# Kernel optimization log

Measured on AMD Instinct MI355X. Metric: run time of the kernel, lower is better.

The kernel has to match this reference:

```python
import jax, jax.numpy as jnp
import numpy as np

B, C, H, W = 4, 3, 256, 256
NCC = 64            # num_conv_channels
N_HIDDEN = 20 - 2   # hidden_block applied num_hiddel_blocks-2 times (shared weights)
EPS = 1e-5          # BatchNorm eps (eval mode: running stats; Dropout2d is identity in eval)


def _bayer_mask():
    # RGGB Bayer pattern: each channel sampled only at its sites, zeros elsewhere
    m = np.zeros((3, H, W), dtype=np.float32)
    m[0, 0::2, 0::2] = 1.0  # R
    m[1, 0::2, 1::2] = 1.0  # G
    m[1, 1::2, 0::2] = 1.0  # G
    m[2, 1::2, 1::2] = 1.0  # B
    return jnp.asarray(m)


def setup_inputs() -> dict:
    key = jax.random.key(0)
    ks = jax.random.split(key, 8)
    X = jax.random.uniform(ks[0], (B, C, H, W), dtype=jnp.float32) * _bayer_mask()[None]
    w_in = jax.random.normal(ks[1], (NCC, 3, 3, 3), dtype=jnp.float32) * 0.15
    b_in = jnp.zeros((NCC,), jnp.float32)
    w_h = jax.random.normal(ks[2], (NCC, NCC, 3, 3), dtype=jnp.float32) * 0.04
    b_h = jnp.zeros((NCC,), jnp.float32)
    w_out = jax.random.normal(ks[3], (3, NCC, 3, 3), dtype=jnp.float32) * 0.04
    b_out = jnp.zeros((3,), jnp.float32)
    def bn_params(n):
        return (jnp.ones((n,), jnp.float32), jnp.zeros((n,), jnp.float32),
                jnp.zeros((n,), jnp.float32), jnp.ones((n,), jnp.float32))
    g_in, be_in, m_in, v_in = bn_params(NCC)
    g_h, be_h, m_h, v_h = bn_params(NCC)
    g_out, be_out, m_out, v_out = bn_params(3)
    return dict(X=X, w_in=w_in, b_in=b_in, g_in=g_in, be_in=be_in, m_in=m_in, v_in=v_in,
                w_h=w_h, b_h=b_h, g_h=g_h, be_h=be_h, m_h=m_h, v_h=v_h,
                w_out=w_out, b_out=b_out, g_out=g_out, be_out=be_out, m_out=m_out, v_out=v_out)


def _conv(x, w, b):
    y = jax.lax.conv_general_dilated(x, w, (1, 1), ((1, 1), (1, 1)),
                                     dimension_numbers=('NCHW', 'OIHW', 'NCHW'))
    return y + b[None, :, None, None]


def _bn(x, g, be, m, v):
    scale = (g / jnp.sqrt(v + EPS))[None, :, None, None]
    return (x - m[None, :, None, None]) * scale + be[None, :, None, None]


def _interpolate_zeros(x):
    # Vectorized masked cross-neighbor average at zero sites, dividing by the
    # count of strictly-positive neighbors (zero-padded borders).
    p = jnp.pad(x, ((0, 0), (0, 0), (1, 1), (1, 1)))
    left = p[:, :, 1:-1, :-2]
    right = p[:, :, 1:-1, 2:]
    top = p[:, :, :-2, 1:-1]
    bottom = p[:, :, 2:, 1:-1]
    nb_sum = left + right + top + bottom
    nb_cnt = ((left > 0).astype(x.dtype) + (right > 0).astype(x.dtype)
              + (top > 0).astype(x.dtype) + (bottom > 0).astype(x.dtype))
    mean = jnp.where(nb_cnt > 0, nb_sum / jnp.maximum(nb_cnt, 1.0), 0.0)
    return jnp.where(x == 0, mean, x)


def reference(X, w_in, b_in, g_in, be_in, m_in, v_in,
              w_h, b_h, g_h, be_h, m_h, v_h,
              w_out, b_out, g_out, be_out, m_out, v_out):
    y = jax.nn.selu(_bn(_conv(X, w_in, b_in), g_in, be_in, m_in, v_in))

    def hidden(y, _):
        y = jax.nn.selu(_bn(_conv(y, w_h, b_h), g_h, be_h, m_h, v_h))
        return y, None

    y, _ = jax.lax.scan(hidden, y, None, length=N_HIDDEN)
    y = jax.nn.selu(_bn(_conv(y, w_out, b_out), g_out, be_out, m_out, v_out))
    return y + _interpolate_zeros(X)
```

## Files before the change

### kernel.cpp

```cpp
#include <hip/hip_runtime.h>

#define EPS 1e-5f
#define SELU_L 1.0507009873554805f
#define SELU_A 1.6732632423543772f
#define SELU_LA (SELU_L * SELU_A)

typedef _Float16 half8 __attribute__((ext_vector_type(8)));
typedef _Float16 half4 __attribute__((ext_vector_type(4)));
typedef float floatx4 __attribute__((ext_vector_type(4)));

__device__ __forceinline__ float selu_f(float x) {
    return x > 0.f ? SELU_L * x : SELU_LA * (__expf(x) - 1.f);
}

__device__ __forceinline__ void gload_lds16(const _Float16* g, _Float16* l) {
    __builtin_amdgcn_global_load_lds(
        (const __attribute__((address_space(1))) void*)g,
        (__attribute__((address_space(3))) void*)l, 16, 0, 0);
}

__global__ __launch_bounds__(256) void k_prep(
    const float* __restrict__ w_h, const float* __restrict__ w_in,
    const float* __restrict__ w_out, _Float16* __restrict__ wb_h,
    _Float16* __restrict__ wb_in, _Float16* __restrict__ wb_out,
    _Float16* __restrict__ zp)
{
    int i = blockIdx.x * 256 + threadIdx.x;
    if (i < 256) zp[i] = (_Float16)0.f;
    if (i < 36864) {
        int t = i >> 11;
        int rem = i & 2047;
        int mi = rem >> 9;
        int L = (rem >> 3) & 63;
        int j = i & 7;
        int co = mi * 16 + (L & 15);
        int ci = ((t & 1) << 5) + ((L >> 4) << 3) + j;
        int s = t >> 1;
        wb_h[i] = (_Float16)w_h[(co * 64 + ci) * 9 + s];
    } else if (i < 36864 + 2048) {
        int e = i - 36864;
        int mi = e >> 9;
        int L = (e >> 3) & 63;
        int j = e & 7;
        int co = mi * 16 + (L & 15);
        int k = ((L >> 4) << 3) + j;
        _Float16 val = (_Float16)0.f;
        if (k < 27) {
            int s = k / 3, ci = k - s * 3;
            val = (_Float16)w_in[(co * 3 + ci) * 9 + s];
        }
        wb_in[e] = val;
    } else if (i < 36864 + 2048 + 9216) {
        int e = i - 36864 - 2048;
        int t = e >> 9;
        int L = (e >> 3) & 63;
        int j = e & 7;
        int co = L & 15;
        int ci = ((t & 1) << 5) + ((L >> 4) << 3) + j;
        int s = t >> 1;
        _Float16 val = (_Float16)0.f;
        if (co < 3) val = (_Float16)w_out[(co * 64 + ci) * 9 + s];
        wb_out[e] = val;
    }
}

__global__ __launch_bounds__(256) void k_conv_in_mfma(
    const float* __restrict__ X, const _Float16* __restrict__ wb,
    const float* __restrict__ bconv, const float* __restrict__ g,
    const float* __restrict__ be, const float* __restrict__ bm,
    const float* __restrict__ bv, _Float16* __restrict__ dst)
{
    __shared__ float s_x[3][18][18];
    __shared__ float s_sc[64], s_bs[64];
    const int tid = threadIdx.x;
    const int tau = ((blockIdx.x & 7) << 7) + (blockIdx.x >> 3);
    const int b = tau >> 8, rem = tau & 255;
    const int h0 = (rem >> 4) << 4, w0 = (rem & 15) << 4;

    if (tid < 64) {
        float sc = g[tid] * rsqrtf(bv[tid] + EPS);
        s_sc[tid] = sc;
        s_bs[tid] = (bconv[tid] - bm[tid]) * sc + be[tid];
    }
    for (int idx = tid; idx < 3 * 324; idx += 256) {
        int ci = idx / 324, rem2 = idx - ci * 324;
        int r = rem2 / 18, c = rem2 - r * 18;
        int gh = h0 - 1 + r, gw = w0 - 1 + c;
        float val = 0.f;
        if ((unsigned)gh < 256u && (unsigned)gw < 256u)
            val = X[((b * 3 + ci) << 16) + (gh << 8) + gw];
        s_x[ci][r][c] = val;
    }
    __syncthreads();

    const int wv = tid >> 6, L = tid & 63, quad = L >> 4, l15 = L & 15;
    half8 a[4];
    #pragma unroll
    for (int mi = 0; mi < 4; ++mi)
        a[mi] = *(const half8*)(wb + (mi * 64 + L) * 8);

    floatx4 acc[4][4];
    #pragma unroll
    for (int mi = 0; mi < 4; ++mi)
        #pragma unroll
        for (int ni = 0; ni < 4; ++ni) acc[mi][ni] = (floatx4){0.f, 0.f, 0.f, 0.f};

    #pragma unroll
    for (int ni = 0; ni < 4; ++ni) {
        half8 bfr;
        #pragma unroll
        for (int j = 0; j < 8; ++j) {
            int k = quad * 8 + j;
            float xv = 0.f;
            if (k < 27) {
                int s = k / 3, ci = k - s * 3;
                int kh = s / 3, kw = s - kh * 3;
                xv = s_x[ci][wv * 4 + ni + kh][l15 + kw];
            }
            bfr[j] = (_Float16)xv;
        }
        #pragma unroll
        for (int mi = 0; mi < 4; ++mi)
            acc[mi][ni] = __builtin_amdgcn_mfma_f32_16x16x32_f16(a[mi], bfr, acc[mi][ni], 0, 0, 0);
    }

    _Float16* db = dst + ((size_t)b << 22);
    #pragma unroll
    for (int mi = 0; mi < 4; ++mi) {
        const int cob = mi * 16 + quad * 4;
        floatx4 sc = *(const floatx4*)(&s_sc[cob]);
        floatx4 bs = *(const floatx4*)(&s_bs[cob]);
        #pragma unroll
        for (int ni = 0; ni < 4; ++ni) {
            half4 ov;
            #pragma unroll
            for (int r = 0; r < 4; ++r)
                ov[r] = (_Float16)selu_f(acc[mi][ni][r] * sc[r] + bs[r]);
            const int row = h0 + wv * 4 + ni, col = w0 + l15;
            *(half4*)(db + ((((row << 8) + col) << 6) + cob)) = ov;
        }
    }
}

__global__ __launch_bounds__(1024) void k_hidden_v14(
    const _Float16* __restrict__ src, const _Float16* __restrict__ wb,
    const float* __restrict__ bconv, const float* __restrict__ g,
    const float* __restrict__ be, const float* __restrict__ bm,
    const float* __restrict__ bv, const _Float16* __restrict__ zp,
    _Float16* __restrict__ dst)
{
    __shared__ _Float16 s_w[36864];
    __shared__ _Float16 s_act[2][20992];
    __shared__ float s_sc[64], s_bs[64];
    const int tid = threadIdx.x;
    const int wv = tid >> 6, L = tid & 63, quad = L >> 4, l15 = L & 15;
    const int rh = wv >> 1, mh = wv & 1;

    if (tid < 64) {
        float sc = g[tid] * rsqrtf(bv[tid] + EPS);
        s_sc[tid] = sc;
        s_bs[tid] = (bconv[tid] - bm[tid]) * sc + be[tid];
    }

    #pragma unroll
    for (int k = 0; k < 5; ++k) {
        const int wc = k * 16 + wv;
        if (wc < 72)
            gload_lds16(wb + ((wc << 6) + L) * 8, &s_w[wc << 9]);
    }

    auto stage = [&](int tau, int buf) {
        const int b = tau >> 8, rem = tau & 255;
        const int h0 = (rem >> 4) << 4, w0 = (rem & 15) << 4;
        const _Float16* sb = src + ((size_t)b << 22);
        #pragma unroll
        for (int k = 0; k < 3; ++k) {
            const int wc = k * 16 + wv;
            if (wc < 41) {
                const int p = (wc << 3) + (L >> 3);
                const int sd = (L & 7) ^ (p & 7);
                const int rp = p / 18, cl = p - rp * 18;
                const int gh = h0 - 1 + rp, gw = w0 - 1 + cl;
                const _Float16* gp = (p < 324 && (unsigned)gh < 256u && (unsigned)gw < 256u)
                    ? sb + ((((gh << 8) + gw) << 6) + (sd << 3)) : zp;
                gload_lds16(gp, &s_act[buf][wc << 9]);
            }
        }
    };

    const int swz = ((blockIdx.x & 7) << 5) + (blockIdx.x >> 3);
    const int tau0 = swz << 2;
    stage(tau0, 0);
    __syncthreads();

    for (int ti = 0; ti < 4; ++ti) {
        const int tau = tau0 + ti, cur = ti & 1;
        if (ti < 3) stage(tau + 1, cur ^ 1);

        floatx4 acc[2][2];
        #pragma unroll
        for (int m = 0; m < 2; ++m)
            #pragma unroll
            for (int ni = 0; ni < 2; ++ni) acc[m][ni] = (floatx4){0.f, 0.f, 0.f, 0.f};

        const _Float16* bufp = &s_act[cur][0];
        #pragma unroll
        for (int h = 0; h < 2; ++h) {
            const int sb8 = (h << 2) + quad;
            #pragma unroll
            for (int kw = 0; kw < 3; ++kw) {
                half8 ac[3][2];
                #pragma unroll
                for (int kh = 0; kh < 3; ++kh) {
                    const int t = ((kh * 3 + kw) << 1) + h;
                    ac[kh][0] = *(const half8*)(&s_w[((t * 4 + mh * 2 + 0) * 64 + L) * 8]);
                    ac[kh][1] = *(const half8*)(&s_w[((t * 4 + mh * 2 + 1) * 64 + L) * 8]);
                }
                #pragma unroll
                for (int j = 0; j < 4; ++j) {
                    const int p = (rh * 2 + j) * 18 + l15 + kw;
                    half8 bfr = *(const half8*)(bufp + (p << 6) + (((p & 7) ^ sb8) << 3));
                    #pragma unroll
                    for (int kh = 0; kh < 3; ++kh) {
                        const int ni = j - kh;
                        if (ni >= 0 && ni < 2) {
                            acc[0][ni] = __builtin_amdgcn_mfma_f32_16x16x32_f16(ac[kh][0], bfr, acc[0][ni], 0, 0, 0);
                            acc[1][ni] = __builtin_amdgcn_mfma_f32_16x16x32_f16(ac[kh][1], bfr, acc[1][ni], 0, 0, 0);
                        }
                    }
                }
            }
        }

        const int b = tau >> 8, rem = tau & 255;
        const int h0 = (rem >> 4) << 4, w0 = (rem & 15) << 4;
        _Float16* db = dst + ((size_t)b << 22);
        #pragma unroll
        for (int m = 0; m < 2; ++m) {
            const int cob = (mh * 2 + m) * 16 + quad * 4;
            floatx4 sc = *(const floatx4*)(&s_sc[cob]);
            floatx4 bs = *(const floatx4*)(&s_bs[cob]);
            #pragma unroll
            for (int ni = 0; ni < 2; ++ni) {
                half4 ov;
                #pragma unroll
                for (int r = 0; r < 4; ++r)
                    ov[r] = (_Float16)selu_f(acc[m][ni][r] * sc[r] + bs[r]);
                const int row = h0 + rh * 2 + ni, col = w0 + l15;
                *(half4*)(db + ((((row << 8) + col) << 6) + cob)) = ov;
            }
        }
        __syncthreads();
    }
}

__global__ __launch_bounds__(256) void k_conv_out_mfma(
    const _Float16* __restrict__ src, const _Float16* __restrict__ wb,
    const float* __restrict__ bconv, const float* __restrict__ g,
    const float* __restrict__ be, const float* __restrict__ bm,
    const float* __restrict__ bv, const float* __restrict__ X,
    float* __restrict__ out)
{
    __shared__ _Float16 s_in[324 * 72];
    const int tid = threadIdx.x;
    const int tau = ((blockIdx.x & 7) << 7) + (blockIdx.x >> 3);
    const int b = tau >> 8, rem = tau & 255;
    const int h0 = (rem >> 4) << 4, w0 = (rem & 15) << 4;
    const _Float16* sb = src + ((size_t)b << 22);

    for (int idx = tid; idx < 2592; idx += 256) {
        int r = idx / 144, cpos = idx - r * 144;
        int col = cpos >> 3, sub = cpos & 7;
        int gh = h0 - 1 + r, gw = w0 - 1 + col;
        half8 val = {0, 0, 0, 0, 0, 0, 0, 0};
        if ((unsigned)gh < 256u && (unsigned)gw < 256u)
            val = *(const half8*)(sb + ((((gh << 8) + gw) << 6) + (sub << 3)));
        *(half8*)(&s_in[(r * 18 + col) * 72 + (sub << 3)]) = val;
    }
    __syncthreads();

    const int wv = tid >> 6, L = tid & 63, quad = L >> 4, l15 = L & 15;
    floatx4 acc[4];
    #pragma unroll
    for (int ni = 0; ni < 4; ++ni) acc[ni] = (floatx4){0.f, 0.f, 0.f, 0.f};

    #pragma unroll
    for (int t = 0; t < 18; ++t) {
        const int s = t >> 1, ci0 = (t & 1) << 5;
        const int kh = s / 3, kw = s - kh * 3;
        half8 a = *(const half8*)(wb + (t * 64 + L) * 8);
        #pragma unroll
        for (int ni = 0; ni < 4; ++ni) {
            const int row = wv * 4 + ni + kh, col = l15 + kw;
            half8 bfr = *(const half8*)(&s_in[(row * 18 + col) * 72 + ci0 + quad * 8]);
            acc[ni] = __builtin_amdgcn_mfma_f32_16x16x32_f16(a, bfr, acc[ni], 0, 0, 0);
        }
    }

    if (quad == 0) {
        float sc[3], bs[3];
        #pragma unroll
        for (int co = 0; co < 3; ++co) {
            sc[co] = g[co] * rsqrtf(bv[co] + EPS);
            bs[co] = (bconv[co] - bm[co]) * sc[co] + be[co];
        }
        #pragma unroll
        for (int ni = 0; ni < 4; ++ni) {
            const int h = h0 + wv * 4 + ni, wc = w0 + l15;
            #pragma unroll
            for (int co = 0; co < 3; ++co) {
                float val = selu_f(acc[ni][co] * sc[co] + bs[co]);
                const float* Xc = X + ((size_t)(b * 3 + co) << 16);
                float x = Xc[(h << 8) + wc];
                float res;
                if (x == 0.f) {
                    float lft = (wc > 0)   ? Xc[(h << 8) + wc - 1] : 0.f;
                    float rgt = (wc < 255) ? Xc[(h << 8) + wc + 1] : 0.f;
                    float top = (h > 0)    ? Xc[((h - 1) << 8) + wc] : 0.f;
                    float bot = (h < 255)  ? Xc[((h + 1) << 8) + wc] : 0.f;
                    float sm = lft + rgt + top + bot;
                    int cnt = (lft > 0.f) + (rgt > 0.f) + (top > 0.f) + (bot > 0.f);
                    res = cnt > 0 ? sm / (float)cnt : 0.f;
                } else {
                    res = x;
                }
                out[((b * 3 + co) << 16) + (h << 8) + wc] = val + res;
            }
        }
    }
}

extern "C" void kernel_launch(void* const* d_in, const int* in_sizes, int n_in,
                              void* d_out, int out_size, void* d_ws, size_t ws_size,
                              hipStream_t stream) {
    (void)in_sizes; (void)n_in; (void)out_size; (void)ws_size;
    const float* X    = (const float*)d_in[0];
    const float* w_in = (const float*)d_in[1];
    const float* b_in = (const float*)d_in[2];
    const float* g_in = (const float*)d_in[3];
    const float* be_in= (const float*)d_in[4];
    const float* m_in = (const float*)d_in[5];
    const float* v_in = (const float*)d_in[6];
    const float* w_h  = (const float*)d_in[7];
    const float* b_h  = (const float*)d_in[8];
    const float* g_h  = (const float*)d_in[9];
    const float* be_h = (const float*)d_in[10];
    const float* m_h  = (const float*)d_in[11];
    const float* v_h  = (const float*)d_in[12];
    const float* w_o  = (const float*)d_in[13];
    const float* b_o  = (const float*)d_in[14];
    const float* g_o  = (const float*)d_in[15];
    const float* be_o = (const float*)d_in[16];
    const float* m_o  = (const float*)d_in[17];
    const float* v_o  = (const float*)d_in[18];
    float* out = (float*)d_out;

    _Float16* act0  = (_Float16*)d_ws;
    _Float16* act1  = act0 + ((size_t)1 << 24);
    _Float16* wb_h  = act1 + ((size_t)1 << 24);
    _Float16* wb_in = wb_h + 36864;
    _Float16* wb_out= wb_in + 2048;
    _Float16* zp    = wb_out + 9216;

    k_prep<<<188, 256, 0, stream>>>(w_h, w_in, w_o, wb_h, wb_in, wb_out, zp);
    k_conv_in_mfma<<<1024, 256, 0, stream>>>(X, wb_in, b_in, g_in, be_in, m_in, v_in, act0);
    _Float16* src = act0;
    _Float16* dst = act1;
    for (int i = 0; i < 18; ++i) {
        k_hidden_v14<<<256, 1024, 0, stream>>>(src, wb_h, b_h, g_h, be_h, m_h, v_h, zp, dst);
        _Float16* t = src; src = dst; dst = t;
    }
    k_conv_out_mfma<<<1024, 256, 0, stream>>>(src, wb_out, b_o, g_o, be_o, m_o, v_o, X, out);
}
```

Measured before the change: 553.2 us.

## Split hidden conv per output-channel half, one tile per block, 2 blocks/CU

Replaces the persistent 1024-thread hidden-layer kernel, which looped over four tiles with double-buffered LDS staging, with 2048 blocks of 512 threads. Each block handles one 16x16 tile and one half of the 64 output channels, so it loads only half the weights. Less LDS per block allows two resident blocks per CU, hiding load latency through occupancy rather than explicit double buffering. In exchange, each input tile halo is now staged twice (once per channel half), and weights are loaded per block, which raises global and L2 traffic.

```diff
diff --git a/kernel.cpp b/kernel.cpp
--- a/kernel.cpp
+++ b/kernel.cpp
@@ -142,19 +142,26 @@
     }
 }
 
-__global__ __launch_bounds__(1024) void k_hidden_v14(
+__global__ __launch_bounds__(512, 2) void k_hidden_v15(
     const _Float16* __restrict__ src, const _Float16* __restrict__ wb,
     const float* __restrict__ bconv, const float* __restrict__ g,
     const float* __restrict__ be, const float* __restrict__ bm,
     const float* __restrict__ bv, const _Float16* __restrict__ zp,
     _Float16* __restrict__ dst)
 {
-    __shared__ _Float16 s_w[36864];
-    __shared__ _Float16 s_act[2][20992];
+    __shared__ _Float16 s_w[18432];
+    __shared__ _Float16 s_act[20992];
     __shared__ float s_sc[64], s_bs[64];
     const int tid = threadIdx.x;
     const int wv = tid >> 6, L = tid & 63, quad = L >> 4, l15 = L & 15;
-    const int rh = wv >> 1, mh = wv & 1;
+    const int rq = wv;
+
+    const int xcd = blockIdx.x & 7, q = blockIdx.x >> 3;
+    const int hb = q & 1;
+    const int tau = (xcd << 7) + (q >> 1);
+    const int b = tau >> 8, rem = tau & 255;
+    const int h0 = (rem >> 4) << 4, w0 = (rem & 15) << 4;
+    const _Float16* sb = src + ((size_t)b << 22);
 
     if (tid < 64) {
         float sc = g[tid] * rsqrtf(bv[tid] + EPS);
@@ -164,93 +171,78 @@
 
     #pragma unroll
     for (int k = 0; k < 5; ++k) {
-        const int wc = k * 16 + wv;
-        if (wc < 72)
-            gload_lds16(wb + ((wc << 6) + L) * 8, &s_w[wc << 9]);
-    }
-
-    auto stage = [&](int tau, int buf) {
-        const int b = tau >> 8, rem = tau & 255;
-        const int h0 = (rem >> 4) << 4, w0 = (rem & 15) << 4;
-        const _Float16* sb = src + ((size_t)b << 22);
-        #pragma unroll
-        for (int k = 0; k < 3; ++k) {
-            const int wc = k * 16 + wv;
-            if (wc < 41) {
-                const int p = (wc << 3) + (L >> 3);
-                const int sd = (L & 7) ^ (p & 7);
-                const int rp = p / 18, cl = p - rp * 18;
-                const int gh = h0 - 1 + rp, gw = w0 - 1 + cl;
-                const _Float16* gp = (p < 324 && (unsigned)gh < 256u && (unsigned)gw < 256u)
-                    ? sb + ((((gh << 8) + gw) << 6) + (sd << 3)) : zp;
-                gload_lds16(gp, &s_act[buf][wc << 9]);
+        const int wcl = k * 8 + wv;
+        if (wcl < 36) {
+            const int t = wcl >> 1, m = wcl & 1;
+            const int wcg = (t << 2) + (hb << 1) + m;
+            gload_lds16(wb + ((wcg << 6) + L) * 8, &s_w[wcl << 9]);
+        }
+    }
+
+    #pragma unroll
+    for (int k = 0; k < 6; ++k) {
+        const int wc = k * 8 + wv;
+        if (wc < 41) {
+            const int p = (wc << 3) + (L >> 3);
+            const int sd = (L & 7) ^ (p & 7);
+            const int rp = p / 18, cl = p - rp * 18;
+            const int gh = h0 - 1 + rp, gw = w0 - 1 + cl;
+            const _Float16* gp = (p < 324 && (unsigned)gh < 256u && (unsigned)gw < 256u)
+                ? sb + ((((gh << 8) + gw) << 6) + (sd << 3)) : zp;
+            gload_lds16(gp, &s_act[wc << 9]);
+        }
+    }
+    __syncthreads();
+
+    floatx4 acc[2][2];
+    #pragma unroll
+    for (int m = 0; m < 2; ++m)
+        #pragma unroll
+        for (int ni = 0; ni < 2; ++ni) acc[m][ni] = (floatx4){0.f, 0.f, 0.f, 0.f};
+
+    #pragma unroll
+    for (int h = 0; h < 2; ++h) {
+        const int sb8 = (h << 2) + quad;
+        #pragma unroll
+        for (int kw = 0; kw < 3; ++kw) {
+            half8 ac[3][2];
+            #pragma unroll
+            for (int kh = 0; kh < 3; ++kh) {
+                const int t = ((kh * 3 + kw) << 1) + h;
+                ac[kh][0] = *(const half8*)(&s_w[((t * 2 + 0) * 64 + L) * 8]);
+                ac[kh][1] = *(const half8*)(&s_w[((t * 2 + 1) * 64 + L) * 8]);
             }
-        }
-    };
-
-    const int swz = ((blockIdx.x & 7) << 5) + (blockIdx.x >> 3);
-    const int tau0 = swz << 2;
-    stage(tau0, 0);
-    __syncthreads();
-
-    for (int ti = 0; ti < 4; ++ti) {
-        const int tau = tau0 + ti, cur = ti & 1;
-        if (ti < 3) stage(tau + 1, cur ^ 1);
-
-        floatx4 acc[2][2];
-        #pragma unroll
-        for (int m = 0; m < 2; ++m)
-            #pragma unroll
-            for (int ni = 0; ni < 2; ++ni) acc[m][ni] = (floatx4){0.f, 0.f, 0.f, 0.f};
-
-        const _Float16* bufp = &s_act[cur][0];
-        #pragma unroll
-        for (int h = 0; h < 2; ++h) {
-            const int sb8 = (h << 2) + quad;
-            #pragma unroll
-            for (int kw = 0; kw < 3; ++kw) {
-                half8 ac[3][2];
+            #pragma unroll
+            for (int j = 0; j < 4; ++j) {
+                const int p = (rq * 2 + j) * 18 + l15 + kw;
+                half8 bfr = *(const half8*)(&s_act[(p << 6) + (((p & 7) ^ sb8) << 3)]);
                 #pragma unroll
                 for (int kh = 0; kh < 3; ++kh) {
-                    const int t = ((kh * 3 + kw) << 1) + h;
-                    ac[kh][0] = *(const half8*)(&s_w[((t * 4 + mh * 2 + 0) * 64 + L) * 8]);
-                    ac[kh][1] = *(const half8*)(&s_w[((t * 4 + mh * 2 + 1) * 64 + L) * 8]);
-                }
-                #pragma unroll
-                for (int j = 0; j < 4; ++j) {
-                    const int p = (rh * 2 + j) * 18 + l15 + kw;
-                    half8 bfr = *(const half8*)(bufp + (p << 6) + (((p & 7) ^ sb8) << 3));
-                    #pragma unroll
-                    for (int kh = 0; kh < 3; ++kh) {
-                        const int ni = j - kh;
-                        if (ni >= 0 && ni < 2) {
-                            acc[0][ni] = __builtin_amdgcn_mfma_f32_16x16x32_f16(ac[kh][0], bfr, acc[0][ni], 0, 0, 0);
-                            acc[1][ni] = __builtin_amdgcn_mfma_f32_16x16x32_f16(ac[kh][1], bfr, acc[1][ni], 0, 0, 0);
-                        }
+                    const int ni = j - kh;
+                    if (ni >= 0 && ni < 2) {
+                        acc[0][ni] = __builtin_amdgcn_mfma_f32_16x16x32_f16(ac[kh][0], bfr, acc[0][ni], 0, 0, 0);
+                        acc[1][ni] = __builtin_amdgcn_mfma_f32_16x16x32_f16(ac[kh][1], bfr, acc[1][ni], 0, 0, 0);
                     }
                 }
             }
         }
-
-        const int b = tau >> 8, rem = tau & 255;
-        const int h0 = (rem >> 4) << 4, w0 = (rem & 15) << 4;
-        _Float16* db = dst + ((size_t)b << 22);
-        #pragma unroll
-        for (int m = 0; m < 2; ++m) {
-            const int cob = (mh * 2 + m) * 16 + quad * 4;
-            floatx4 sc = *(const floatx4*)(&s_sc[cob]);
-            floatx4 bs = *(const floatx4*)(&s_bs[cob]);
-            #pragma unroll
-            for (int ni = 0; ni < 2; ++ni) {
-                half4 ov;
-                #pragma unroll
-                for (int r = 0; r < 4; ++r)
-                    ov[r] = (_Float16)selu_f(acc[m][ni][r] * sc[r] + bs[r]);
-                const int row = h0 + rh * 2 + ni, col = w0 + l15;
-                *(half4*)(db + ((((row << 8) + col) << 6) + cob)) = ov;
-            }
-        }
-        __syncthreads();
+    }
+
+    _Float16* db = dst + ((size_t)b << 22);
+    #pragma unroll
+    for (int m = 0; m < 2; ++m) {
+        const int cob = ((hb << 1) + m) * 16 + quad * 4;
+        floatx4 sc = *(const floatx4*)(&s_sc[cob]);
+        floatx4 bs = *(const floatx4*)(&s_bs[cob]);
+        #pragma unroll
+        for (int ni = 0; ni < 2; ++ni) {
+            half4 ov;
+            #pragma unroll
+            for (int r = 0; r < 4; ++r)
+                ov[r] = (_Float16)selu_f(acc[m][ni][r] * sc[r] + bs[r]);
+            const int row = h0 + rq * 2 + ni, col = w0 + l15;
+            *(half4*)(db + ((((row << 8) + col) << 6) + cob)) = ov;
+        }
     }
 }
 
@@ -367,7 +359,7 @@
     _Float16* src = act0;
     _Float16* dst = act1;
     for (int i = 0; i < 18; ++i) {
-        k_hidden_v14<<<256, 1024, 0, stream>>>(src, wb_h, b_h, g_h, be_h, m_h, v_h, zp, dst);
+        k_hidden_v15<<<2048, 512, 0, stream>>>(src, wb_h, b_h, g_h, be_h, m_h, v_h, zp, dst);
         _Float16* t = src; src = dst; dst = t;
     }
     k_conv_out_mfma<<<1024, 256, 0, stream>>>(src, wb_out, b_o, g_o, be_o, m_o, v_o, X, out);
```

Result: slower. 607.9 us (+9.9%).
